# Optimization experiments

Measured on AMD Instinct MI355X. Metric: run time of the kernel, lower is better.

The kernel has to match this reference:

```python
import jax, jax.numpy as jnp
import numpy as np

N_HEADS = 12
HEAD_DIM = 64
EMB = 768


def setup_inputs() -> dict:
    key = jax.random.key(0)
    k1, k2, k3 = jax.random.split(key, 3)
    B, S = 4, 2048
    x = jax.random.normal(k1, (B, S, EMB), dtype=jnp.float32)
    # nn.Linear-style init scale ~ 1/sqrt(fan_in)
    w_qkv = jax.random.normal(k2, (EMB, 3 * N_HEADS * HEAD_DIM), dtype=jnp.float32) * (EMB ** -0.5)
    w_out = jax.random.normal(k3, (N_HEADS * HEAD_DIM, EMB), dtype=jnp.float32) * ((N_HEADS * HEAD_DIM) ** -0.5)
    b_out = jnp.zeros((EMB,), dtype=jnp.float32)
    return {"x": x, "w_qkv": w_qkv, "w_out": w_out, "b_out": b_out}


def reference(x, w_qkv, w_out, b_out):
    B, S, E = x.shape
    qkv = x @ w_qkv                                   # [B,S,3*H*D]
    q, k, v = jnp.split(qkv, 3, axis=-1)
    def to_heads(t):
        return t.reshape(B, S, N_HEADS, HEAD_DIM).transpose(0, 2, 1, 3)  # [B,H,S,D]
    q, k, v = to_heads(q), to_heads(k), to_heads(v)
    scores = jnp.einsum('bhqd,bhkd->bhqk', q, k) / (HEAD_DIM ** 0.5)     # [B,H,S,S]
    probs = jax.nn.softmax(scores, axis=-1)
    attn = jnp.einsum('bhqk,bhkd->bhqd', probs, v)                       # [B,H,S,D]
    attn = attn.transpose(0, 2, 1, 3).reshape(B, S, N_HEADS * HEAD_DIM)
    return attn @ w_out + b_out
```

## Files before the change

kernel.cpp:

```cpp
#include <hip/hip_runtime.h>
#include <stdint.h>

typedef unsigned short u16;
typedef __attribute__((ext_vector_type(8))) __bf16 bf16x8;
typedef __attribute__((ext_vector_type(4))) __bf16 bf16x4;
typedef __attribute__((ext_vector_type(8))) unsigned short u16x8;
typedef __attribute__((ext_vector_type(4))) float f32x4;

__device__ __forceinline__ void glds16(const u16* g, u16* l) {
  auto* gp = reinterpret_cast<const __attribute__((address_space(1))) unsigned*>(
      reinterpret_cast<uintptr_t>(g));
  auto* lp = reinterpret_cast<__attribute__((address_space(3))) unsigned*>(
      reinterpret_cast<uintptr_t>(l));
  __builtin_amdgcn_global_load_lds(gp, lp, 16, 0, 0);
}

__device__ __forceinline__ void tp_tile(const float* __restrict__ src,
                                        u16* __restrict__ dst, int C, int Rd,
                                        int r0, int c0, float scale, u16* lds) {
  const int tid = threadIdx.x;
  {
    int r = tid >> 2, cb = (tid & 3) * 16;
#pragma unroll
    for (int k = 0; k < 4; ++k) {
      f32x4 v = *(const f32x4*)&src[(long)(r0 + r) * C + c0 + cb + k * 4];
      v = v * scale;
      *(bf16x4*)&lds[r * 72 + cb + k * 4] = __builtin_convertvector(v, bf16x4);
    }
  }
  __syncthreads();
  {
    int c = tid >> 2, rb = (tid & 3) * 16;
    u16x8 o0, o1;
#pragma unroll
    for (int q = 0; q < 8; ++q) {
      o0[q] = lds[(rb + q) * 72 + c];
      o1[q] = lds[(rb + 8 + q) * 72 + c];
    }
    *(u16x8*)&dst[(long)(c0 + c) * Rd + r0 + rb] = o0;
    *(u16x8*)&dst[(long)(c0 + c) * Rd + r0 + rb + 8] = o1;
  }
}

__global__ __launch_bounds__(256) void prep_k(const float* __restrict__ w_qkv,
                                              const float* __restrict__ w_out,
                                              const float* __restrict__ x,
                                              u16* __restrict__ wqkvT,
                                              u16* __restrict__ woutT,
                                              u16* __restrict__ xb) {
  __shared__ u16 lds[64 * 72];
  int bx = blockIdx.x;
  if (bx < 432) {
    int tr = bx / 36, tc = bx % 36;
    float sc = (tc < 12) ? 0.18033688011112042f : 1.0f;
    tp_tile(w_qkv, wqkvT, 2304, 768, tr * 64, tc * 64, sc, lds);
  } else if (bx < 576) {
    int t = bx - 432;
    tp_tile(w_out, woutT, 768, 768, (t / 12) * 64, (t % 12) * 64, 1.0f, lds);
  } else {
    int base = ((bx - 576) * 256 + (int)threadIdx.x) * 8;
#pragma unroll
    for (int it = 0; it < 16; ++it, base += 393216) {
      f32x4 a = *(const f32x4*)&x[base];
      f32x4 b = *(const f32x4*)&x[base + 4];
      *(bf16x4*)&xb[base] = __builtin_convertvector(a, bf16x4);
      *(bf16x4*)&xb[base + 4] = __builtin_convertvector(b, bf16x4);
    }
  }
}

template <bool OF32>
__device__ __forceinline__ void gemm_core(const u16* __restrict__ A,
                                          const u16* __restrict__ BT,
                                          void* __restrict__ Cv,
                                          const float* __restrict__ bias,
                                          int N, int K, int br, int bc,
                                          u16* As, u16* Bs) {
  const int tid = threadIdx.x;
  const int lane = tid & 63, wave = tid >> 6;
  const int quad = lane >> 4, l16 = lane & 15;
  const int wm = (wave >> 1) * 64, wn = (wave & 1) * 64;

  f32x4 acc[4][4] = {};

  const int srow = wave * 32 + (lane >> 2);
  const int scol = ((lane & 3) ^ ((lane >> 3) & 3)) * 8;
  const u16* ag = A + (long)(br + srow) * K + scol;
  const u16* bg = BT + (long)(bc + srow) * K + scol;
  const int rd = (quad ^ ((l16 >> 1) & 3)) * 8;

  for (int k0 = 0; k0 < K; k0 += 32) {
    glds16(ag + k0, As + wave * 1024);
    glds16(ag + k0 + 16 * K, As + wave * 1024 + 512);
    glds16(bg + k0, Bs + wave * 1024);
    glds16(bg + k0 + 16 * K, Bs + wave * 1024 + 512);
    __syncthreads();
    bf16x8 af[4], bf[4];
#pragma unroll
    for (int i = 0; i < 4; ++i)
      af[i] = *(const bf16x8*)&As[(wm + i * 16 + l16) * 32 + rd];
#pragma unroll
    for (int j = 0; j < 4; ++j)
      bf[j] = *(const bf16x8*)&Bs[(wn + j * 16 + l16) * 32 + rd];
#pragma unroll
    for (int i = 0; i < 4; ++i)
#pragma unroll
      for (int j = 0; j < 4; ++j)
        acc[i][j] = __builtin_amdgcn_mfma_f32_16x16x32_bf16(af[i], bf[j],
                                                            acc[i][j], 0, 0, 0);
    __syncthreads();
  }

#pragma unroll
  for (int i = 0; i < 4; ++i)
#pragma unroll
    for (int j = 0; j < 4; ++j)
#pragma unroll
      for (int r = 0; r < 4; ++r) {
        int row = br + wm + i * 16 + quad * 4 + r;
        int col = bc + wn + j * 16 + l16;
        float v = acc[i][j][r];
        if (OF32) {
          ((float*)Cv)[(long)row * N + col] = v + bias[col];
        } else {
          ((__bf16*)Cv)[(long)row * N + col] = (__bf16)v;
        }
      }
}

__global__ __launch_bounds__(256) void qkvt_k(const u16* __restrict__ xb,
                                              const u16* __restrict__ wqkvT,
                                              u16* __restrict__ qk,
                                              u16* __restrict__ vt) {
  __shared__ __align__(16) u16 As[128 * 32];
  __shared__ __align__(16) u16 Bs[128 * 32];
  int bx = blockIdx.x;
  if (bx < 768) {
    gemm_core<false>(xb, wqkvT, qk, nullptr, 1536, 768, (bx / 12) * 128,
                     (bx % 12) * 128, As, Bs);
  } else {
    int i = bx - 768;
    gemm_core<false>(wqkvT + 1536 * 768, xb, vt, nullptr, 8192, 768,
                     (i >> 6) * 128, (i & 63) * 128, As, Bs);
  }
}

__global__ __launch_bounds__(256) void gemm2_k(const u16* __restrict__ attnb,
                                               const u16* __restrict__ woutT,
                                               float* __restrict__ out,
                                               const float* __restrict__ bias) {
  __shared__ __align__(16) u16 As[128 * 32];
  __shared__ __align__(16) u16 Bs[128 * 32];
  gemm_core<true>(attnb, woutT, out, bias, 768, 768, blockIdx.y * 128,
                  blockIdx.x * 128, As, Bs);
}

__global__ __launch_bounds__(256, 3) void attn_k(const u16* __restrict__ qk,
                                                 const u16* __restrict__ vt,
                                                 u16* __restrict__ attnb) {
  const int LQ = 72;
  __shared__ __align__(16) u16 smem[17408];
  u16* Ks = smem;
  u16* Vs = smem + 4096;
  u16* Ps = smem + 8192;

  const int tid = threadIdx.x;
  const int lane = tid & 63, wave = tid >> 6;
  const int quad = lane >> 4, l16 = lane & 15;
  const int qh = wave >> 1, sh = wave & 1;
  const int bid = blockIdx.x;
  const int xcd = bid & 7, slot = bid >> 3;
  const int bh = xcd * 6 + (slot >> 4);
  const int qt = slot & 15;
  const int bloc = bh / 12, h = bh % 12;
  const long rowbase = (long)bloc * 2048;

#pragma unroll
  for (int it = 0; it < 4; ++it) {
    int c = tid + it * 256;
    int m = c >> 3, off = (c & 7) * 8;
    *(u16x8*)&Ps[m * LQ + off] =
        *(const u16x8*)&qk[(rowbase + qt * 128 + m) * 1536 + h * 64 + off];
  }
  __syncthreads();

  bf16x8 aq[2][4];
#pragma unroll
  for (int kk = 0; kk < 2; ++kk)
#pragma unroll
    for (int i = 0; i < 4; ++i)
      aq[kk][i] = *(const bf16x8*)&Ps[(qh * 64 + i * 16 + l16) * LQ + kk * 32 +
                                      quad * 8];

  bf16x8 ones;
#pragma unroll
  for (int q = 0; q < 8; ++q) ones[q] = (__bf16)1.0f;

  const int trow = lane >> 3;
  const int tcol = ((lane & 7) ^ trow) * 8;
  const u16* kg = qk + (rowbase + wave * 16 + trow) * 1536 + 768 + h * 64 + tcol;
  const u16* vg = vt + (long)(h * 64 + wave * 16 + trow) * 8192 + rowbase + tcol;
  u16* kl = Ks + wave * 1024;
  u16* vl = Vs + wave * 1024;
  const int sw = l16 & 7;

  f32x4 o[4][4] = {};
  f32x4 l_acc[4] = {};

  for (int t = 0; t < 32; ++t) {
    const long kvK = (long)t * 64 * 1536;
    const long kvV = (long)t * 64;
    glds16(kg + kvK, kl);
    glds16(kg + kvK + 8 * 1536, kl + 512);
    glds16(vg + kvV, vl);
    glds16(vg + kvV + 8 * 8192, vl + 512);
    __syncthreads();

#pragma unroll
    for (int j = 0; j < 2; ++j) {
      bf16x8 bk0 = *(const bf16x8*)&Ks[(sh * 32 + j * 16 + l16) * 64 +
                                       ((0 * 4 + quad) ^ sw) * 8];
      bf16x8 bk1 = *(const bf16x8*)&Ks[(sh * 32 + j * 16 + l16) * 64 +
                                       ((1 * 4 + quad) ^ sw) * 8];
      f32x4 sc[4] = {};
#pragma unroll
      for (int i = 0; i < 4; ++i) {
        sc[i] = __builtin_amdgcn_mfma_f32_16x16x32_bf16(bk0, aq[0][i], sc[i],
                                                        0, 0, 0);
        sc[i] = __builtin_amdgcn_mfma_f32_16x16x32_bf16(bk1, aq[1][i], sc[i],
                                                        0, 0, 0);
      }
#pragma unroll
      for (int i = 0; i < 4; ++i) {
        f32x4 p;
#pragma unroll
        for (int r = 0; r < 4; ++r) p[r] = exp2f(sc[i][r]);
        *(bf16x4*)&Ps[(qh * 64 + i * 16 + l16) * LQ + sh * 32 + j * 16 +
                      quad * 4] = __builtin_convertvector(p, bf16x4);
      }
    }

    {
      bf16x8 bv[4];
#pragma unroll
      for (int n = 0; n < 4; ++n)
        bv[n] = *(const bf16x8*)&Vs[(n * 16 + l16) * 64 +
                                    ((sh * 4 + quad) ^ sw) * 8];
#pragma unroll
      for (int i = 0; i < 4; ++i) {
        bf16x8 ap = *(const bf16x8*)&Ps[(qh * 64 + i * 16 + l16) * LQ +
                                        sh * 32 + quad * 8];
        l_acc[i] = __builtin_amdgcn_mfma_f32_16x16x32_bf16(ones, ap, l_acc[i],
                                                           0, 0, 0);
#pragma unroll
        for (int n = 0; n < 4; ++n)
          o[i][n] = __builtin_amdgcn_mfma_f32_16x16x32_bf16(ap, bv[n], o[i][n],
                                                            0, 0, 0);
      }
    }
    __syncthreads();
  }

  float* Of = (float*)smem;
  float* Lp = (float*)&smem[16384];
  if (sh == 1) {
#pragma unroll
    for (int i = 0; i < 4; ++i) {
#pragma unroll
      for (int n = 0; n < 4; ++n)
#pragma unroll
        for (int r = 0; r < 4; ++r)
          Of[(qh * 64 + i * 16 + quad * 4 + r) * 64 + n * 16 + l16] =
              o[i][n][r];
      if (quad == 0) Lp[qh * 64 + i * 16 + l16] = l_acc[i][0];
    }
  }
  __syncthreads();
  if (sh == 0) {
#pragma unroll
    for (int i = 0; i < 4; ++i) {
      float lsum = l_acc[i][0] + Lp[qh * 64 + i * 16 + l16];
      f32x4 inv;
#pragma unroll
      for (int r = 0; r < 4; ++r)
        inv[r] = 1.0f / __shfl(lsum, quad * 4 + r, 64);
#pragma unroll
      for (int n = 0; n < 4; ++n)
#pragma unroll
        for (int r = 0; r < 4; ++r) {
          int srow = qt * 128 + qh * 64 + i * 16 + quad * 4 + r;
          float v = o[i][n][r] +
                    Of[(qh * 64 + i * 16 + quad * 4 + r) * 64 + n * 16 + l16];
          ((__bf16*)attnb)[(rowbase + srow) * 768 + h * 64 + n * 16 + l16] =
              (__bf16)(v * inv[r]);
        }
    }
  }
}

extern "C" void kernel_launch(void* const* d_in, const int* in_sizes, int n_in,
                              void* d_out, int out_size, void* d_ws,
                              size_t ws_size, hipStream_t stream) {
  const float* x = (const float*)d_in[0];
  const float* w_qkv = (const float*)d_in[1];
  const float* w_out = (const float*)d_in[2];
  const float* b_out = (const float*)d_in[3];
  float* out = (float*)d_out;

  char* ws = (char*)d_ws;
  u16* wqkvT = (u16*)(ws);
  u16* woutT = (u16*)(ws + 3538944);
  u16* vt = (u16*)(ws + 4718592);
  u16* xb = (u16*)(ws + 17301504);
  u16* attnb = xb;
  u16* qkb = (u16*)d_out;

  prep_k<<<768, 256, 0, stream>>>(w_qkv, w_out, x, wqkvT, woutT, xb);
  qkvt_k<<<1152, 256, 0, stream>>>(xb, wqkvT, qkb, vt);
  attn_k<<<768, 256, 0, stream>>>(qkb, vt, attnb);
  gemm2_k<<<dim3(6, 64), 256, 0, stream>>>(attnb, woutT, out, b_out);
}
```

Before: 229.2 us.

## Double-buffer LDS tiles in GEMM and attention kernels with prefetch and setprio

Converts the GEMM core and the attention KV loop to double-buffered LDS. The next tile's global-to-LDS loads are issued before the current tile is computed, and each iteration ends with a single barrier that also waits on outstanding memory counters. MFMA sections are wrapped in s_setprio, and exp2f is replaced with the hardware exp2 builtin. The cost is roughly doubled LDS per block, which can lower occupancy, especially for the attention kernel with launch bounds of 3 blocks.

```diff
diff --git a/kernel.cpp b/kernel.cpp
--- a/kernel.cpp
+++ b/kernel.cpp
@@ -13,6 +13,12 @@
   auto* lp = reinterpret_cast<__attribute__((address_space(3))) unsigned*>(
       reinterpret_cast<uintptr_t>(l));
   __builtin_amdgcn_global_load_lds(gp, lp, 16, 0, 0);
+}
+
+__device__ __forceinline__ void pipe_bar() {
+  asm volatile("s_waitcnt vmcnt(0) lgkmcnt(0)" ::: "memory");
+  __builtin_amdgcn_s_barrier();
+  asm volatile("" ::: "memory");
 }
 
 __device__ __forceinline__ void tp_tile(const float* __restrict__ src,
@@ -89,26 +95,43 @@
   const u16* bg = BT + (long)(bc + srow) * K + scol;
   const int rd = (quad ^ ((l16 >> 1) & 3)) * 8;
 
-  for (int k0 = 0; k0 < K; k0 += 32) {
-    glds16(ag + k0, As + wave * 1024);
-    glds16(ag + k0 + 16 * K, As + wave * 1024 + 512);
-    glds16(bg + k0, Bs + wave * 1024);
-    glds16(bg + k0 + 16 * K, Bs + wave * 1024 + 512);
-    __syncthreads();
+  glds16(ag, As + wave * 1024);
+  glds16(ag + 16 * K, As + wave * 1024 + 512);
+  glds16(bg, Bs + wave * 1024);
+  glds16(bg + 16 * K, Bs + wave * 1024 + 512);
+  pipe_bar();
+
+  const int nk = K / 32;
+#pragma unroll 2
+  for (int kt = 0; kt < nk; ++kt) {
+    const int pb = kt & 1;
+    const u16* asc = As + pb * 4096;
+    const u16* bsc = Bs + pb * 4096;
+    if (kt + 1 < nk) {
+      u16* asn = As + (pb ^ 1) * 4096;
+      u16* bsn = Bs + (pb ^ 1) * 4096;
+      const int k0 = (kt + 1) * 32;
+      glds16(ag + k0, asn + wave * 1024);
+      glds16(ag + k0 + 16 * K, asn + wave * 1024 + 512);
+      glds16(bg + k0, bsn + wave * 1024);
+      glds16(bg + k0 + 16 * K, bsn + wave * 1024 + 512);
+    }
     bf16x8 af[4], bf[4];
 #pragma unroll
     for (int i = 0; i < 4; ++i)
-      af[i] = *(const bf16x8*)&As[(wm + i * 16 + l16) * 32 + rd];
+      af[i] = *(const bf16x8*)&asc[(wm + i * 16 + l16) * 32 + rd];
 #pragma unroll
     for (int j = 0; j < 4; ++j)
-      bf[j] = *(const bf16x8*)&Bs[(wn + j * 16 + l16) * 32 + rd];
+      bf[j] = *(const bf16x8*)&bsc[(wn + j * 16 + l16) * 32 + rd];
+    __builtin_amdgcn_s_setprio(1);
 #pragma unroll
     for (int i = 0; i < 4; ++i)
 #pragma unroll
       for (int j = 0; j < 4; ++j)
         acc[i][j] = __builtin_amdgcn_mfma_f32_16x16x32_bf16(af[i], bf[j],
                                                             acc[i][j], 0, 0, 0);
-    __syncthreads();
+    __builtin_amdgcn_s_setprio(0);
+    pipe_bar();
   }
 
 #pragma unroll
@@ -132,8 +155,8 @@
                                               const u16* __restrict__ wqkvT,
                                               u16* __restrict__ qk,
                                               u16* __restrict__ vt) {
-  __shared__ __align__(16) u16 As[128 * 32];
-  __shared__ __align__(16) u16 Bs[128 * 32];
+  __shared__ __align__(16) u16 As[2 * 128 * 32];
+  __shared__ __align__(16) u16 Bs[2 * 128 * 32];
   int bx = blockIdx.x;
   if (bx < 768) {
     gemm_core<false>(xb, wqkvT, qk, nullptr, 1536, 768, (bx / 12) * 128,
@@ -149,8 +172,8 @@
                                                const u16* __restrict__ woutT,
                                                float* __restrict__ out,
                                                const float* __restrict__ bias) {
-  __shared__ __align__(16) u16 As[128 * 32];
-  __shared__ __align__(16) u16 Bs[128 * 32];
+  __shared__ __align__(16) u16 As[2 * 128 * 32];
+  __shared__ __align__(16) u16 Bs[2 * 128 * 32];
   gemm_core<true>(attnb, woutT, out, bias, 768, 768, blockIdx.y * 128,
                   blockIdx.x * 128, As, Bs);
 }
@@ -159,10 +182,8 @@
                                                  const u16* __restrict__ vt,
                                                  u16* __restrict__ attnb) {
   const int LQ = 72;
-  __shared__ __align__(16) u16 smem[17408];
-  u16* Ks = smem;
-  u16* Vs = smem + 4096;
-  u16* Ps = smem + 8192;
+  __shared__ __align__(16) u16 smem[16384 + 9216];
+  u16* Ps = smem + 16384;
 
   const int tid = threadIdx.x;
   const int lane = tid & 63, wave = tid >> 6;
@@ -175,6 +196,16 @@
   const int bloc = bh / 12, h = bh % 12;
   const long rowbase = (long)bloc * 2048;
 
+  const int trow = lane >> 3;
+  const int tcol = ((lane & 7) ^ trow) * 8;
+  const u16* kg = qk + (rowbase + wave * 16 + trow) * 1536 + 768 + h * 64 + tcol;
+  const u16* vg = vt + (long)(h * 64 + wave * 16 + trow) * 8192 + rowbase + tcol;
+
+  glds16(kg, smem + wave * 1024);
+  glds16(kg + 8 * 1536, smem + wave * 1024 + 512);
+  glds16(vg, smem + 8192 + wave * 1024);
+  glds16(vg + 8 * 8192, smem + 8192 + wave * 1024 + 512);
+
 #pragma unroll
   for (int it = 0; it < 4; ++it) {
     int c = tid + it * 256;
@@ -196,33 +227,34 @@
 #pragma unroll
   for (int q = 0; q < 8; ++q) ones[q] = (__bf16)1.0f;
 
-  const int trow = lane >> 3;
-  const int tcol = ((lane & 7) ^ trow) * 8;
-  const u16* kg = qk + (rowbase + wave * 16 + trow) * 1536 + 768 + h * 64 + tcol;
-  const u16* vg = vt + (long)(h * 64 + wave * 16 + trow) * 8192 + rowbase + tcol;
-  u16* kl = Ks + wave * 1024;
-  u16* vl = Vs + wave * 1024;
   const int sw = l16 & 7;
-
   f32x4 o[4][4] = {};
   f32x4 l_acc[4] = {};
 
+#pragma unroll 2
   for (int t = 0; t < 32; ++t) {
-    const long kvK = (long)t * 64 * 1536;
-    const long kvV = (long)t * 64;
-    glds16(kg + kvK, kl);
-    glds16(kg + kvK + 8 * 1536, kl + 512);
-    glds16(vg + kvV, vl);
-    glds16(vg + kvV + 8 * 8192, vl + 512);
-    __syncthreads();
+    const int pb = t & 1;
+    const u16* ksc = smem + pb * 4096;
+    const u16* vsc = smem + 8192 + pb * 4096;
+    if (t < 31) {
+      u16* ksn = smem + (pb ^ 1) * 4096;
+      u16* vsn = smem + 8192 + (pb ^ 1) * 4096;
+      const long kvK = (long)(t + 1) * 64 * 1536;
+      const long kvV = (long)(t + 1) * 64;
+      glds16(kg + kvK, ksn + wave * 1024);
+      glds16(kg + kvK + 8 * 1536, ksn + wave * 1024 + 512);
+      glds16(vg + kvV, vsn + wave * 1024);
+      glds16(vg + kvV + 8 * 8192, vsn + wave * 1024 + 512);
+    }
 
 #pragma unroll
     for (int j = 0; j < 2; ++j) {
-      bf16x8 bk0 = *(const bf16x8*)&Ks[(sh * 32 + j * 16 + l16) * 64 +
-                                       ((0 * 4 + quad) ^ sw) * 8];
-      bf16x8 bk1 = *(const bf16x8*)&Ks[(sh * 32 + j * 16 + l16) * 64 +
-                                       ((1 * 4 + quad) ^ sw) * 8];
+      bf16x8 bk0 = *(const bf16x8*)&ksc[(sh * 32 + j * 16 + l16) * 64 +
+                                        (quad ^ sw) * 8];
+      bf16x8 bk1 = *(const bf16x8*)&ksc[(sh * 32 + j * 16 + l16) * 64 +
+                                        ((4 + quad) ^ sw) * 8];
       f32x4 sc[4] = {};
+      __builtin_amdgcn_s_setprio(1);
 #pragma unroll
       for (int i = 0; i < 4; ++i) {
         sc[i] = __builtin_amdgcn_mfma_f32_16x16x32_bf16(bk0, aq[0][i], sc[i],
@@ -230,11 +262,13 @@
         sc[i] = __builtin_amdgcn_mfma_f32_16x16x32_bf16(bk1, aq[1][i], sc[i],
                                                         0, 0, 0);
       }
+      __builtin_amdgcn_s_setprio(0);
 #pragma unroll
       for (int i = 0; i < 4; ++i) {
         f32x4 p;
 #pragma unroll
-        for (int r = 0; r < 4; ++r) p[r] = exp2f(sc[i][r]);
+        for (int r = 0; r < 4; ++r)
+          p[r] = __builtin_amdgcn_exp2f(sc[i][r]);
         *(bf16x4*)&Ps[(qh * 64 + i * 16 + l16) * LQ + sh * 32 + j * 16 +
                       quad * 4] = __builtin_convertvector(p, bf16x4);
       }
@@ -244,8 +278,9 @@
       bf16x8 bv[4];
 #pragma unroll
       for (int n = 0; n < 4; ++n)
-        bv[n] = *(const bf16x8*)&Vs[(n * 16 + l16) * 64 +
-                                    ((sh * 4 + quad) ^ sw) * 8];
+        bv[n] = *(const bf16x8*)&vsc[(n * 16 + l16) * 64 +
+                                     ((sh * 4 + quad) ^ sw) * 8];
+      __builtin_amdgcn_s_setprio(1);
 #pragma unroll
       for (int i = 0; i < 4; ++i) {
         bf16x8 ap = *(const bf16x8*)&Ps[(qh * 64 + i * 16 + l16) * LQ +
@@ -257,8 +292,10 @@
           o[i][n] = __builtin_amdgcn_mfma_f32_16x16x32_bf16(ap, bv[n], o[i][n],
                                                             0, 0, 0);
       }
-    }
-    __syncthreads();
+      __builtin_amdgcn_s_setprio(0);
+    }
+
+    pipe_bar();
   }
 
   float* Of = (float*)smem;
```

Result: faster. 215.5 us (-6.0%).

## Shrink attention query tile, double-buffer V and prefetch K across iterations

Applied to the files above, without the earlier changes.

The attention kernel now handles 64 query rows per block instead of 128 and launches twice as many blocks. Q fragments are loaded straight from global memory instead of staged through LDS. V is double-buffered and the next K tile is prefetched after the score phase, with explicit waitcnt barriers in place of __syncthreads. The P buffer switches to an XOR-swizzled 64-wide layout, and occupancy hints rise to 4 blocks/SM. The aim is to hide global-load latency and raise occupancy, at the cost of reloading K/V twice as often per query.

```diff
diff --git a/kernel.cpp b/kernel.cpp
--- a/kernel.cpp
+++ b/kernel.cpp
@@ -13,6 +13,18 @@
   auto* lp = reinterpret_cast<__attribute__((address_space(3))) unsigned*>(
       reinterpret_cast<uintptr_t>(l));
   __builtin_amdgcn_global_load_lds(gp, lp, 16, 0, 0);
+}
+
+__device__ __forceinline__ void pipe_bar() {
+  asm volatile("s_waitcnt vmcnt(0) lgkmcnt(0)" ::: "memory");
+  __builtin_amdgcn_s_barrier();
+  asm volatile("" ::: "memory");
+}
+
+__device__ __forceinline__ void lds_bar() {
+  asm volatile("s_waitcnt lgkmcnt(0)" ::: "memory");
+  __builtin_amdgcn_s_barrier();
+  asm volatile("" ::: "memory");
 }
 
 __device__ __forceinline__ void tp_tile(const float* __restrict__ src,
@@ -155,14 +167,13 @@
                   blockIdx.x * 128, As, Bs);
 }
 
-__global__ __launch_bounds__(256, 3) void attn_k(const u16* __restrict__ qk,
+__global__ __launch_bounds__(256, 4) void attn_k(const u16* __restrict__ qk,
                                                  const u16* __restrict__ vt,
                                                  u16* __restrict__ attnb) {
-  const int LQ = 72;
-  __shared__ __align__(16) u16 smem[17408];
+  __shared__ __align__(16) u16 smem[16384];
   u16* Ks = smem;
   u16* Vs = smem + 4096;
-  u16* Ps = smem + 8192;
+  u16* Ps = smem + 12288;
 
   const int tid = threadIdx.x;
   const int lane = tid & 63, wave = tid >> 6;
@@ -170,86 +181,98 @@
   const int qh = wave >> 1, sh = wave & 1;
   const int bid = blockIdx.x;
   const int xcd = bid & 7, slot = bid >> 3;
-  const int bh = xcd * 6 + (slot >> 4);
-  const int qt = slot & 15;
+  const int bh = xcd * 6 + (slot >> 5);
+  const int qt = slot & 31;
   const int bloc = bh / 12, h = bh % 12;
   const long rowbase = (long)bloc * 2048;
-
-#pragma unroll
-  for (int it = 0; it < 4; ++it) {
-    int c = tid + it * 256;
-    int m = c >> 3, off = (c & 7) * 8;
-    *(u16x8*)&Ps[m * LQ + off] =
-        *(const u16x8*)&qk[(rowbase + qt * 128 + m) * 1536 + h * 64 + off];
-  }
-  __syncthreads();
-
-  bf16x8 aq[2][4];
-#pragma unroll
-  for (int kk = 0; kk < 2; ++kk)
-#pragma unroll
-    for (int i = 0; i < 4; ++i)
-      aq[kk][i] = *(const bf16x8*)&Ps[(qh * 64 + i * 16 + l16) * LQ + kk * 32 +
-                                      quad * 8];
-
-  bf16x8 ones;
-#pragma unroll
-  for (int q = 0; q < 8; ++q) ones[q] = (__bf16)1.0f;
 
   const int trow = lane >> 3;
   const int tcol = ((lane & 7) ^ trow) * 8;
   const u16* kg = qk + (rowbase + wave * 16 + trow) * 1536 + 768 + h * 64 + tcol;
   const u16* vg = vt + (long)(h * 64 + wave * 16 + trow) * 8192 + rowbase + tcol;
   u16* kl = Ks + wave * 1024;
-  u16* vl = Vs + wave * 1024;
+
+  glds16(kg, kl);
+  glds16(kg + 8 * 1536, kl + 512);
+  glds16(vg, Vs + wave * 1024);
+  glds16(vg + 8 * 8192, Vs + wave * 1024 + 512);
+
+  bf16x8 aq[2][2];
+#pragma unroll
+  for (int kk = 0; kk < 2; ++kk)
+#pragma unroll
+    for (int i = 0; i < 2; ++i)
+      aq[kk][i] = *(const bf16x8*)&qk[(rowbase + qt * 64 + qh * 32 + i * 16 +
+                                       l16) * 1536 + h * 64 + kk * 32 +
+                                      quad * 8];
+
+  bf16x8 ones;
+#pragma unroll
+  for (int q = 0; q < 8; ++q) ones[q] = (__bf16)1.0f;
+
   const int sw = l16 & 7;
-
-  f32x4 o[4][4] = {};
-  f32x4 l_acc[4] = {};
+  f32x4 o[2][4] = {};
+  f32x4 l_acc[2] = {};
+
+  pipe_bar();
 
   for (int t = 0; t < 32; ++t) {
-    const long kvK = (long)t * 64 * 1536;
-    const long kvV = (long)t * 64;
-    glds16(kg + kvK, kl);
-    glds16(kg + kvK + 8 * 1536, kl + 512);
-    glds16(vg + kvV, vl);
-    glds16(vg + kvV + 8 * 8192, vl + 512);
-    __syncthreads();
+    const int pb = t & 1;
+    const u16* vsc = Vs + pb * 4096;
+
+    if (t < 31) {
+      u16* vsn = Vs + (pb ^ 1) * 4096;
+      const long kvV = (long)(t + 1) * 64;
+      glds16(vg + kvV, vsn + wave * 1024);
+      glds16(vg + kvV + 8 * 8192, vsn + wave * 1024 + 512);
+    }
 
 #pragma unroll
     for (int j = 0; j < 2; ++j) {
       bf16x8 bk0 = *(const bf16x8*)&Ks[(sh * 32 + j * 16 + l16) * 64 +
-                                       ((0 * 4 + quad) ^ sw) * 8];
+                                       (quad ^ sw) * 8];
       bf16x8 bk1 = *(const bf16x8*)&Ks[(sh * 32 + j * 16 + l16) * 64 +
-                                       ((1 * 4 + quad) ^ sw) * 8];
-      f32x4 sc[4] = {};
-#pragma unroll
-      for (int i = 0; i < 4; ++i) {
+                                       ((4 + quad) ^ sw) * 8];
+      f32x4 sc[2] = {};
+#pragma unroll
+      for (int i = 0; i < 2; ++i) {
         sc[i] = __builtin_amdgcn_mfma_f32_16x16x32_bf16(bk0, aq[0][i], sc[i],
                                                         0, 0, 0);
         sc[i] = __builtin_amdgcn_mfma_f32_16x16x32_bf16(bk1, aq[1][i], sc[i],
                                                         0, 0, 0);
       }
 #pragma unroll
-      for (int i = 0; i < 4; ++i) {
+      for (int i = 0; i < 2; ++i) {
         f32x4 p;
 #pragma unroll
-        for (int r = 0; r < 4; ++r) p[r] = exp2f(sc[i][r]);
-        *(bf16x4*)&Ps[(qh * 64 + i * 16 + l16) * LQ + sh * 32 + j * 16 +
-                      quad * 4] = __builtin_convertvector(p, bf16x4);
+        for (int r = 0; r < 4; ++r)
+          p[r] = __builtin_amdgcn_exp2f(sc[i][r]);
+        const int prow = qh * 32 + i * 16 + l16;
+        const int pchunk = (sh * 4 + j * 2 + (quad >> 1)) ^ (l16 & 7);
+        *(bf16x4*)&Ps[prow * 64 + pchunk * 8 + (quad & 1) * 4] =
+            __builtin_convertvector(p, bf16x4);
       }
+    }
+
+    lds_bar();
+
+    if (t < 31) {
+      const long kvK = (long)(t + 1) * 64 * 1536;
+      glds16(kg + kvK, kl);
+      glds16(kg + kvK + 8 * 1536, kl + 512);
     }
 
     {
       bf16x8 bv[4];
 #pragma unroll
       for (int n = 0; n < 4; ++n)
-        bv[n] = *(const bf16x8*)&Vs[(n * 16 + l16) * 64 +
-                                    ((sh * 4 + quad) ^ sw) * 8];
-#pragma unroll
-      for (int i = 0; i < 4; ++i) {
-        bf16x8 ap = *(const bf16x8*)&Ps[(qh * 64 + i * 16 + l16) * LQ +
-                                        sh * 32 + quad * 8];
+        bv[n] = *(const bf16x8*)&vsc[(n * 16 + l16) * 64 +
+                                     ((sh * 4 + quad) ^ sw) * 8];
+#pragma unroll
+      for (int i = 0; i < 2; ++i) {
+        const int prow = qh * 32 + i * 16 + l16;
+        const int pchunk = (sh * 4 + quad) ^ (l16 & 7);
+        bf16x8 ap = *(const bf16x8*)&Ps[prow * 64 + pchunk * 8];
         l_acc[i] = __builtin_amdgcn_mfma_f32_16x16x32_bf16(ones, ap, l_acc[i],
                                                            0, 0, 0);
 #pragma unroll
@@ -258,28 +281,29 @@
                                                             0, 0, 0);
       }
     }
-    __syncthreads();
+
+    pipe_bar();
   }
 
   float* Of = (float*)smem;
-  float* Lp = (float*)&smem[16384];
+  float* Lp = (float*)(smem + 8192);
   if (sh == 1) {
 #pragma unroll
-    for (int i = 0; i < 4; ++i) {
+    for (int i = 0; i < 2; ++i) {
 #pragma unroll
       for (int n = 0; n < 4; ++n)
 #pragma unroll
         for (int r = 0; r < 4; ++r)
-          Of[(qh * 64 + i * 16 + quad * 4 + r) * 64 + n * 16 + l16] =
+          Of[(qh * 32 + i * 16 + quad * 4 + r) * 64 + n * 16 + l16] =
               o[i][n][r];
-      if (quad == 0) Lp[qh * 64 + i * 16 + l16] = l_acc[i][0];
+      if (quad == 0) Lp[qh * 32 + i * 16 + l16] = l_acc[i][0];
     }
   }
   __syncthreads();
   if (sh == 0) {
 #pragma unroll
-    for (int i = 0; i < 4; ++i) {
-      float lsum = l_acc[i][0] + Lp[qh * 64 + i * 16 + l16];
+    for (int i = 0; i < 2; ++i) {
+      float lsum = l_acc[i][0] + Lp[qh * 32 + i * 16 + l16];
       f32x4 inv;
 #pragma unroll
       for (int r = 0; r < 4; ++r)
@@ -288,9 +312,9 @@
       for (int n = 0; n < 4; ++n)
 #pragma unroll
         for (int r = 0; r < 4; ++r) {
-          int srow = qt * 128 + qh * 64 + i * 16 + quad * 4 + r;
+          int srow = qt * 64 + qh * 32 + i * 16 + quad * 4 + r;
           float v = o[i][n][r] +
-                    Of[(qh * 64 + i * 16 + quad * 4 + r) * 64 + n * 16 + l16];
+                    Of[(qh * 32 + i * 16 + quad * 4 + r) * 64 + n * 16 + l16];
           ((__bf16*)attnb)[(rowbase + srow) * 768 + h * 64 + n * 16 + l16] =
               (__bf16)(v * inv[r]);
         }
@@ -317,6 +341,6 @@
 
   prep_k<<<768, 256, 0, stream>>>(w_qkv, w_out, x, wqkvT, woutT, xb);
   qkvt_k<<<1152, 256, 0, stream>>>(xb, wqkvT, qkb, vt);
-  attn_k<<<768, 256, 0, stream>>>(qkb, vt, attnb);
+  attn_k<<<1536, 256, 0, stream>>>(qkb, vt, attnb);
   gemm2_k<<<dim3(6, 64), 256, 0, stream>>>(attnb, woutT, out, b_out);
 }
```

Result: faster. 217.0 us (-5.3%).
